# Performance work log

Hardware: AMD Instinct MI355X
Metric: run time of the kernel (lower is better)

The kernel has to match this reference:

```python
import jax, jax.numpy as jnp
import numpy as np
from jax import lax

N, C, H, W = 16, 512, 64, 64
INTER, HEADS, GROUPS, K = 512, 64, 8, 7
HEAD_DIM = INTER // HEADS


def setup_inputs() -> dict:
    key = jax.random.key(0)
    ks = jax.random.split(key, 12)
    s = 0.02
    return {
        "x": jax.random.normal(ks[0], (N, C, H, W), jnp.float32),
        "conv_w": jax.random.normal(ks[1], (INTER, C // GROUPS, K, K), jnp.float32) * s,
        "conv_b": jax.random.normal(ks[2], (INTER,), jnp.float32) * s,
        "ln_g": jnp.ones((INTER,), jnp.float32),
        "ln_b": jnp.zeros((INTER,), jnp.float32),
        "qw": jax.random.normal(ks[3], (INTER, INTER), jnp.float32) * s,
        "qb": jax.random.normal(ks[4], (INTER,), jnp.float32) * s,
        "kw": jax.random.normal(ks[5], (INTER, INTER), jnp.float32) * s,
        "kb": jax.random.normal(ks[6], (INTER,), jnp.float32) * s,
        "vw": jax.random.normal(ks[7], (INTER, INTER), jnp.float32) * s,
        "vb": jax.random.normal(ks[8], (INTER,), jnp.float32) * s,
        "pw": jax.random.normal(ks[9], (C, INTER), jnp.float32) * s,
        "pb": jax.random.normal(ks[10], (C,), jnp.float32) * s,
        "beta": jax.random.normal(ks[11], (1,), jnp.float32),
    }


def reference(x, conv_w, conv_b, ln_g, ln_b, qw, qb, kw, kb, vw, vb, pw, pb, beta):
    n, c, h, w = x.shape
    hw = h * w
    pad = (K - 1) // 2
    # grouped conv, NCHW
    xc = lax.conv_general_dilated(
        x, conv_w, window_strides=(1, 1), padding=[(pad, pad), (pad, pad)],
        dimension_numbers=("NCHW", "OIHW", "NCHW"), feature_group_count=GROUPS)
    xc = xc + conv_b[None, :, None, None]
    xc = xc.reshape(n, INTER, hw).transpose(0, 2, 1)  # [N, HW, INTER]
    # LayerNorm over channel dim
    mu = jnp.mean(xc, axis=-1, keepdims=True)
    var = jnp.mean(jnp.square(xc - mu), axis=-1, keepdims=True)
    xn = (xc - mu) * lax.rsqrt(var + 1e-5) * ln_g + ln_b
    # projections (torch Linear: y = x @ W.T + b)
    q = (xn @ qw.T + qb).reshape(n, hw, HEADS, HEAD_DIM).transpose(0, 2, 1, 3)  # [N,h,HW,d]
    k = (xn @ kw.T + kb).reshape(n, hw, HEADS, HEAD_DIM).transpose(0, 2, 3, 1)  # [N,h,d,HW]
    v = (xn @ vw.T + vb).reshape(n, hw, HEADS, HEAD_DIM).transpose(0, 2, 1, 3)  # [N,h,HW,d]
    k = jax.nn.softmax(k, axis=3)  # softmax over tokens
    corr = jnp.einsum("nhds,nhse->nhde", k, v)      # [N,h,d,d] compact context
    atten = jnp.einsum("nhsd,nhde->nhse", q, corr)  # [N,h,HW,d]
    atten = atten.transpose(0, 2, 1, 3).reshape(n, hw, INTER)
    xa = (atten @ pw.T + pb).transpose(0, 2, 1).reshape(n, c, h, w)
    return beta[0] * xa + x
```

## Files before the change

### kernel.cpp

```cpp
#include <hip/hip_runtime.h>
#include <hip/hip_bf16.h>

#define N_IMG 16
#define C_DIM 512
#define H_DIM 64
#define W_DIM 64
#define HW 4096
#define INTER 512
#define HEADS 64
#define GROUPS 8
#define KSZ 7
#define CPG 64
#define M_TOT (N_IMG * HW)

typedef short bf16x8 __attribute__((ext_vector_type(8)));
typedef short bf16x4 __attribute__((ext_vector_type(4)));
typedef float f32x4 __attribute__((ext_vector_type(4)));
typedef unsigned int u32;

__device__ __forceinline__ unsigned short f2bf(float f) {
    __hip_bfloat16 h = __float2bfloat16(f);
    return *reinterpret_cast<unsigned short*>(&h);
}
__device__ __forceinline__ float bf2f(unsigned short u) {
    u32 x = ((u32)u) << 16;
    union { u32 i; float f; } c; c.i = x; return c.f;
}
__device__ __forceinline__ void gload16(const void* g, void* l) {
    __builtin_amdgcn_global_load_lds(
        (const __attribute__((address_space(1))) u32*)g,
        (__attribute__((address_space(3))) u32*)l, 16, 0, 0);
}

__global__ __launch_bounds__(256) void zero_kernel(float* __restrict__ p)
{
    p[blockIdx.x * 256 + threadIdx.x] = 0.f;
}

__global__ __launch_bounds__(256) void wpack_kernel(
    const float* __restrict__ cw, unsigned short* __restrict__ pk)
{
    int p = blockIdx.x * 256 + threadIdx.x;
    int ci = p & 63;
    int co = (p >> 6) & 63;
    int r  = p >> 12;
    int dx = r % 7;
    int dyg = r / 7;
    int dy = dyg % 7;
    int g  = dyg / 7;
    float v = cw[(((size_t)(g * 64 + co)) * 64 + ci) * 49 + dy * 7 + dx];
    pk[(size_t)(g * 49 + dy * 7 + dx) * 4096 + co * 64 + (ci ^ ((co & 7) << 3))] = f2bf(v);
}

__global__ __launch_bounds__(256) void wpack_proj_kernel(
    const float* __restrict__ w, unsigned short* __restrict__ wp)
{
    int e = blockIdx.x * 256 + threadIdx.x;
    int j = e & 7;
    int chunk = (e >> 3) & 511;
    int kt = (e >> 12) & 15;
    int t = e >> 16;
    int col = chunk & 127, kq = chunk >> 7;
    wp[e] = f2bf(w[(size_t)(t * 128 + col) * 512 + kt * 32 + kq * 8 + j]);
}

__global__ __launch_bounds__(256) void pwcast_kernel(
    const float* __restrict__ w, unsigned short* __restrict__ wb)
{
    int i = blockIdx.x * 256 + threadIdx.x;
    wb[i] = f2bf(w[i]);
}

__global__ __launch_bounds__(256) void xprep_kernel(
    const float* __restrict__ x, unsigned short* __restrict__ xb)
{
    const int row = blockIdx.x;
    const int g   = blockIdx.y;
    const int n   = blockIdx.z;
    const int tid = threadIdx.x;
    unsigned short* dst = xb + ((size_t)(n * 8 + g) * 70 + row) * 4608;

    if (row < 3 || row > 66) {
        bf16x8 z = (bf16x8){0,0,0,0,0,0,0,0};
        *(bf16x8*)&dst[tid * 8] = z;
        *(bf16x8*)&dst[(256 + tid) * 8] = z;
        if (tid < 64) *(bf16x8*)&dst[(512 + tid) * 8] = z;
        return;
    }
    const int y = row - 3;
    const int xcol = tid & 63;
    const int oct = tid >> 6;
    const int col = xcol + 3;
    const int cswz = (col & 7) << 3;
    const float* src = x + (((size_t)(n * C_DIM + g * CPG)) * H_DIM + y) * W_DIM + xcol;
#pragma unroll
    for (int h = 0; h < 2; ++h) {
        const int ci0 = oct * 16 + h * 8;
        unsigned short tmp[8];
#pragma unroll
        for (int j = 0; j < 8; ++j)
            tmp[j] = f2bf(src[(size_t)(ci0 + j) * (H_DIM * W_DIM)]);
        *(bf16x8*)&dst[col * 64 + (ci0 ^ cswz)] = *(bf16x8*)tmp;
    }
    if (tid < 64) {
        const int hc[8] = {0, 1, 2, 67, 68, 69, 70, 71};
        int c = hc[tid >> 3], o8 = (tid & 7) * 8;
        *(bf16x8*)&dst[c * 64 + (o8 ^ ((c & 7) << 3))] = (bf16x8){0,0,0,0,0,0,0,0};
    }
}

__global__ __launch_bounds__(256) void conv_mfma2_kernel(
    const unsigned short* __restrict__ xb, const unsigned short* __restrict__ pk,
    const float* __restrict__ cb, unsigned short* __restrict__ xc)
{
    __shared__ __align__(16) unsigned short in_ring[4 * 72 * 64];
    __shared__ __align__(16) unsigned short w_lds[2 * 4096];

    const int bid  = blockIdx.x;
    const int wgid = (bid & 7) * 256 + (bid >> 3);
    const int g  = wgid >> 8;
    const int n  = (wgid >> 4) & 15;
    const int y0 = (wgid & 15) * 4;
    const int tid  = threadIdx.x;
    const int lane = tid & 63;
    const int wv   = tid >> 6;
    const int lx   = lane & 15;
    const int q4   = lane >> 4;
    const int koff = q4 * 8;

    const unsigned short* xbase = xb + ((size_t)(n * 8 + g) * 70) * 4608;
    const unsigned short* pkg   = pk + (size_t)g * 49 * 4096;

    f32x4 acc[4][4];
#pragma unroll
    for (int i = 0; i < 4; ++i)
#pragma unroll
        for (int j = 0; j < 4; ++j) acc[i][j] = (f32x4){0.f, 0.f, 0.f, 0.f};

#pragma unroll
    for (int r = 0; r < 4; ++r) {
        const unsigned short* src = xbase + (size_t)(y0 + r) * 4608;
        gload16(src + tid * 8,         &in_ring[r * 4608 + tid * 8]);
        gload16(src + (256 + tid) * 8, &in_ring[r * 4608 + (256 + tid) * 8]);
        if (tid < 64)
            gload16(src + (512 + tid) * 8, &in_ring[r * 4608 + (512 + tid) * 8]);
    }
    gload16(pkg + tid * 8,         &w_lds[tid * 8]);
    gload16(pkg + (256 + tid) * 8, &w_lds[(256 + tid) * 8]);
    __syncthreads();

    for (int dy = 0; dy < 7; ++dy) {
        if (dy > 0) {
            const int slot = (dy + 3) & 3;
            const unsigned short* src = xbase + (size_t)(y0 + dy + 3) * 4608;
            gload16(src + tid * 8,         &in_ring[slot * 4608 + tid * 8]);
            gload16(src + (256 + tid) * 8, &in_ring[slot * 4608 + (256 + tid) * 8]);
            if (tid < 64)
                gload16(src + (512 + tid) * 8, &in_ring[slot * 4608 + (512 + tid) * 8]);
            __syncthreads();
        }
#pragma unroll
        for (int dx = 0; dx < 7; ++dx) {
            const int t = dy * 7 + dx;
            if (t < 48) {
                const unsigned short* wsrc = pkg + (size_t)(t + 1) * 4096;
                unsigned short* wdst = &w_lds[((t + 1) & 1) * 4096];
                gload16(wsrc + tid * 8,         wdst + tid * 8);
                gload16(wsrc + (256 + tid) * 8, wdst + (256 + tid) * 8);
            }
            const unsigned short* wcur = &w_lds[(t & 1) * 4096];
            bf16x8 b[2][4];
#pragma unroll
            for (int kc = 0; kc < 2; ++kc)
#pragma unroll
                for (int ct = 0; ct < 4; ++ct) {
                    const int co = ct * 16 + lx;
                    b[kc][ct] = *(const bf16x8*)
                        &wcur[co * 64 + ((kc * 32 + koff) ^ ((co & 7) << 3))];
                }
            const int col  = wv * 16 + lx + dx;
            const int cswz = (col & 7) << 3;
#pragma unroll
            for (int ty = 0; ty < 4; ++ty) {
                const int slot = (dy + ty) & 3;
#pragma unroll
                for (int kc = 0; kc < 2; ++kc) {
                    bf16x8 a = *(const bf16x8*)
                        &in_ring[slot * 4608 + col * 64 + ((kc * 32 + koff) ^ cswz)];
#pragma unroll
                    for (int ct = 0; ct < 4; ++ct)
                        acc[ty][ct] = __builtin_amdgcn_mfma_f32_16x16x32_bf16(
                            a, b[kc][ct], acc[ty][ct], 0, 0, 0);
                }
            }
            __syncthreads();
        }
    }

#pragma unroll
    for (int ct = 0; ct < 4; ++ct) {
        const float bv = cb[g * 64 + ct * 16 + lx];
        const int cidx = g * 64 + ct * 16 + lx;
#pragma unroll
        for (int ty = 0; ty < 4; ++ty) {
            const int yy = y0 + ty;
#pragma unroll
            for (int r = 0; r < 4; ++r) {
                const int xx = wv * 16 + q4 * 4 + r;
                xc[((size_t)(n * HW + yy * W_DIM + xx)) * INTER + cidx]
                    = f2bf(acc[ty][ct][r] + bv);
            }
        }
    }
}

__global__ __launch_bounds__(256) void ln_kernel(
    unsigned short* __restrict__ xc, const float* __restrict__ g,
    const float* __restrict__ b)
{
    const int tid  = threadIdx.x;
    const int half = tid >> 7;
    const int l    = tid & 127;
    const size_t row = (size_t)blockIdx.x * 2 + half;

    bf16x4 u = *(const bf16x4*)(xc + row * INTER + l * 4);
    float v0 = bf2f((unsigned short)u[0]), v1 = bf2f((unsigned short)u[1]);
    float v2 = bf2f((unsigned short)u[2]), v3 = bf2f((unsigned short)u[3]);
    float s  = v0 + v1 + v2 + v3;
    float sq = v0 * v0 + v1 * v1 + v2 * v2 + v3 * v3;
#pragma unroll
    for (int off = 32; off; off >>= 1) {
        s  += __shfl_xor(s, off);
        sq += __shfl_xor(sq, off);
    }
    __shared__ float red[4][2];
    const int wid = tid >> 6;
    if ((tid & 63) == 0) { red[wid][0] = s; red[wid][1] = sq; }
    __syncthreads();
    const int w0 = half * 2;
    float S  = red[w0][0] + red[w0 + 1][0];
    float SQ = red[w0][1] + red[w0 + 1][1];
    float mu  = S * (1.f / INTER);
    float var = SQ * (1.f / INTER) - mu * mu;
    float rs  = rsqrtf(var + 1e-5f);
    float4 gg = ((const float4*)g)[l];
    float4 bb = ((const float4*)b)[l];
    bf16x4 o;
    o[0] = (short)f2bf((v0 - mu) * rs * gg.x + bb.x);
    o[1] = (short)f2bf((v1 - mu) * rs * gg.y + bb.y);
    o[2] = (short)f2bf((v2 - mu) * rs * gg.z + bb.z);
    o[3] = (short)f2bf((v3 - mu) * rs * gg.w + bb.w);
    *(bf16x4*)(xc + row * INTER + l * 4) = o;
}

__global__ __launch_bounds__(256, 2) void gemm_kv_corr_kernel(
    const unsigned short* __restrict__ A,
    const unsigned short* __restrict__ Wk, const unsigned short* __restrict__ Wv,
    const float* __restrict__ bk, const float* __restrict__ bv,
    float* __restrict__ crw, float* __restrict__ esw)
{
    __shared__ __align__(16) unsigned short pool[32768];
    unsigned short* ek_lds = pool;
    unsigned short* v_lds  = pool + 16384;

    const int tid  = threadIdx.x;
    const int lane = tid & 63;
    const int w    = tid >> 6;
    const int lx   = lane & 15;
    const int kq4  = lane >> 4;

    const int orig = blockIdx.x;
    const int wgid = (orig & 7) * 256 + (orig >> 3);
    const int m0   = (wgid >> 2) * 128;
    const int ct4  = wgid & 3;
    const int mbase = (w & 1) * 64;
    const int nbase = (w >> 1) * 64;
    const int n = m0 >> 12;

    const unsigned short* wkt = Wk + (size_t)ct4 * 65536;
    const unsigned short* wvt = Wv + (size_t)ct4 * 65536;

    f32x4 acck[4][4], accv[4][4];
#pragma unroll
    for (int i = 0; i < 4; ++i)
#pragma unroll
        for (int j = 0; j < 4; ++j) {
            acck[i][j] = (f32x4){0.f, 0.f, 0.f, 0.f};
            accv[i][j] = (f32x4){0.f, 0.f, 0.f, 0.f};
        }

#pragma unroll
    for (int it = 0; it < 2; ++it) {
        int c = it * 256 + tid;
        gload16(A + (size_t)(m0 + (c & 127)) * 512 + (c >> 7) * 8, &pool[c * 8]);
        gload16(wkt + c * 8, &pool[(1024 + c) * 8]);
        gload16(wvt + c * 8, &pool[(2048 + c) * 8]);
    }
    __syncthreads();

    for (int kt = 0; kt < 16; ++kt) {
        const int b = kt & 1;
        if (kt < 15) {
            const int nb = b ^ 1;
#pragma unroll
            for (int it = 0; it < 2; ++it) {
                int c = it * 256 + tid;
                gload16(A + (size_t)(m0 + (c & 127)) * 512 + (kt + 1) * 32 + (c >> 7) * 8,
                        &pool[(nb * 512 + c) * 8]);
                gload16(wkt + (size_t)(kt + 1) * 4096 + c * 8, &pool[(1024 + nb * 512 + c) * 8]);
                gload16(wvt + (size_t)(kt + 1) * 4096 + c * 8, &pool[(2048 + nb * 512 + c) * 8]);
            }
        }
        bf16x8 a[4], bkf[4], bvf[4];
#pragma unroll
        for (int i = 0; i < 4; ++i) {
            a[i]   = *(const bf16x8*)&pool[(b * 512 + kq4 * 128 + mbase + i * 16 + lx) * 8];
            bkf[i] = *(const bf16x8*)&pool[(1024 + b * 512 + kq4 * 128 + nbase + i * 16 + lx) * 8];
            bvf[i] = *(const bf16x8*)&pool[(2048 + b * 512 + kq4 * 128 + nbase + i * 16 + lx) * 8];
        }
#pragma unroll
        for (int i = 0; i < 4; ++i)
#pragma unroll
            for (int j = 0; j < 4; ++j) {
                acck[i][j] = __builtin_amdgcn_mfma_f32_16x16x32_bf16(a[i], bkf[j], acck[i][j], 0, 0, 0);
                accv[i][j] = __builtin_amdgcn_mfma_f32_16x16x32_bf16(a[i], bvf[j], accv[i][j], 0, 0, 0);
            }
        __syncthreads();
    }

#pragma unroll
    for (int j = 0; j < 4; ++j) {
        const int colk = nbase + j * 16 + lx;
        const float bkv = bk[ct4 * 128 + colk];
        const float bvv = bv[ct4 * 128 + colk];
        const int sw = (colk & 7) << 3;
#pragma unroll
        for (int i = 0; i < 4; ++i) {
            const int t0 = mbase + i * 16 + kq4 * 4;
            const int idx = colk * 128 + (t0 ^ sw);
            bf16x4 ew, vw;
#pragma unroll
            for (int r = 0; r < 4; ++r) {
                ew[r] = (short)f2bf(__expf(acck[i][j][r] + bkv));
                vw[r] = (short)f2bf(accv[i][j][r] + bvv);
            }
            *(bf16x4*)&ek_lds[idx] = ew;
            *(bf16x4*)&v_lds[idx]  = vw;
        }
    }
    const int d = lane >> 3, e = lane & 7;
    const int hbase = (w >> 1) * 8;
#pragma unroll
    for (int h = 0; h < 8; ++h) {
        const int hb = hbase + h;
        const int ck = hb * 8 + d;
        const int ce = hb * 8 + e;
        const int swk = d << 3, swe = e << 3;
        float crh = 0.f, esh = 0.f;
#pragma unroll
        for (int tb = 0; tb < 16; ++tb) {
            const int t0 = mbase + tb * 4;
            bf16x4 ekv = *(const bf16x4*)&ek_lds[ck * 128 + (t0 ^ swk)];
            bf16x4 vvv = *(const bf16x4*)&v_lds[ce * 128 + (t0 ^ swe)];
#pragma unroll
            for (int r = 0; r < 4; ++r) {
                float ekf = bf2f((unsigned short)ekv[r]);
                crh = fmaf(ekf, bf2f((unsigned short)vvv[r]), crh);
                esh += ekf;
            }
        }
        const int nh = n * 64 + ct4 * 16 + hb;
        atomicAdd(&crw[(size_t)nh * 64 + d * 8 + e], crh);
        if (e == 0) atomicAdd(&esw[nh * 8 + d], esh);
    }
}

__global__ __launch_bounds__(256) void norm_corr_kernel(
    const float* __restrict__ crw, const float* __restrict__ esw,
    float* __restrict__ corr)
{
    int idx = blockIdx.x * 256 + threadIdx.x;
    int nh = idx >> 6, d = (idx >> 3) & 7;
    corr[idx] = crw[idx] / esw[nh * 8 + d];
}

__global__ __launch_bounds__(256) void gcomp_kernel(
    const float* __restrict__ qw, const float* __restrict__ corr,
    unsigned short* __restrict__ G)
{
    const int h = blockIdx.x;
    const int n = blockIdx.y;
    const int tid = threadIdx.x;
    __shared__ float C[64];
    if (tid < 64) C[tid] = corr[((size_t)(n * 64 + h)) * 64 + tid];
    __syncthreads();
#pragma unroll
    for (int rep = 0; rep < 2; ++rep) {
        const int k = rep * 256 + tid;
        float o[8] = {};
#pragma unroll
        for (int d = 0; d < 8; ++d) {
            float qv = qw[(size_t)(h * 8 + d) * 512 + k];
#pragma unroll
            for (int e = 0; e < 8; ++e) o[e] = fmaf(qv, C[d * 8 + e], o[e]);
        }
        bf16x8 ov;
#pragma unroll
        for (int e = 0; e < 8; ++e) ov[e] = (short)f2bf(o[e]);
        *(bf16x8*)&G[((size_t)n * 512 + k) * 512 + h * 8] = ov;
    }
}

__global__ __launch_bounds__(256) void compose_kernel(
    const unsigned short* __restrict__ Pwb, const unsigned short* __restrict__ G,
    unsigned short* __restrict__ Wf)
{
    __shared__ __align__(16) unsigned short pool[16384];
    const int tid  = threadIdx.x;
    const int lane = tid & 63;
    const int w    = tid >> 6;
    const int lx   = lane & 15;
    const int kq4  = lane >> 4;

    const int tile = blockIdx.x;
    const int n    = blockIdx.y;
    const int m0 = (tile >> 2) * 128;
    const int n0 = (tile & 3) * 128;
    const int mbase = (w & 1) * 64;
    const int nbase = (w >> 1) * 64;
    const unsigned short* Gn = G + (size_t)n * 262144;

    f32x4 acc[4][4];
#pragma unroll
    for (int i = 0; i < 4; ++i)
#pragma unroll
        for (int j = 0; j < 4; ++j) acc[i][j] = (f32x4){0.f, 0.f, 0.f, 0.f};

#pragma unroll
    for (int it = 0; it < 2; ++it) {
        int c = it * 256 + tid;
        gload16(Pwb + (size_t)(m0 + (c & 127)) * 512 + (c >> 7) * 8, &pool[c * 8]);
        gload16(Gn + (size_t)(n0 + (c & 127)) * 512 + (c >> 7) * 8, &pool[(1024 + c) * 8]);
    }
    __syncthreads();

    for (int kt = 0; kt < 16; ++kt) {
        const int b = kt & 1;
        if (kt < 15) {
            const int nb = b ^ 1;
#pragma unroll
            for (int it = 0; it < 2; ++it) {
                int c = it * 256 + tid;
                gload16(Pwb + (size_t)(m0 + (c & 127)) * 512 + (kt + 1) * 32 + (c >> 7) * 8,
                        &pool[(nb * 512 + c) * 8]);
                gload16(Gn + (size_t)(n0 + (c & 127)) * 512 + (kt + 1) * 32 + (c >> 7) * 8,
                        &pool[(1024 + nb * 512 + c) * 8]);
            }
        }
        bf16x8 a[4], bf[4];
#pragma unroll
        for (int i = 0; i < 4; ++i) {
            a[i]  = *(const bf16x8*)&pool[(b * 512 + kq4 * 128 + mbase + i * 16 + lx) * 8];
            bf[i] = *(const bf16x8*)&pool[(1024 + b * 512 + kq4 * 128 + nbase + i * 16 + lx) * 8];
        }
#pragma unroll
        for (int i = 0; i < 4; ++i)
#pragma unroll
            for (int j = 0; j < 4; ++j)
                acc[i][j] = __builtin_amdgcn_mfma_f32_16x16x32_bf16(a[i], bf[j], acc[i][j], 0, 0, 0);
        __syncthreads();
    }

#pragma unroll
    for (int j = 0; j < 4; ++j) {
        const int col = n0 + nbase + j * 16 + lx;
#pragma unroll
        for (int i = 0; i < 4; ++i) {
            const int rowb = m0 + mbase + i * 16 + kq4 * 4;
#pragma unroll
            for (int r = 0; r < 4; ++r)
                Wf[(size_t)n * 262144 + (size_t)(rowb + r) * 512 + col] = f2bf(acc[i][j][r]);
        }
    }
}

__global__ __launch_bounds__(256) void wfpack_kernel(
    const unsigned short* __restrict__ Wf, unsigned short* __restrict__ wfp)
{
    const int n = blockIdx.y;
    int e = blockIdx.x * 256 + threadIdx.x;
    int j = e & 7;
    int chunk = (e >> 3) & 511;
    int kt = (e >> 12) & 15;
    int t = e >> 16;
    int col = chunk & 127, kq = chunk >> 7;
    wfp[(size_t)n * 262144 + e] =
        Wf[(size_t)n * 262144 + (size_t)(t * 128 + col) * 512 + kt * 32 + kq * 8 + j];
}

__global__ __launch_bounds__(256) void bias2_kernel(
    const float* __restrict__ qb, const float* __restrict__ corr,
    const float* __restrict__ pw, const float* __restrict__ pb,
    float* __restrict__ b2)
{
    const int n = blockIdx.x;
    const int tid = threadIdx.x;
    __shared__ float qbc[512];
#pragma unroll
    for (int rep = 0; rep < 2; ++rep) {
        int j = rep * 256 + tid;
        int h = j >> 3, e = j & 7;
        float s = 0.f;
#pragma unroll
        for (int d = 0; d < 8; ++d)
            s += qb[h * 8 + d] * corr[((size_t)(n * 64 + h)) * 64 + d * 8 + e];
        qbc[j] = s;
    }
    __syncthreads();
#pragma unroll
    for (int rep = 0; rep < 2; ++rep) {
        int c = rep * 256 + tid;
        const float4* pr = (const float4*)(pw + (size_t)c * 512);
        float s = pb[c];
        for (int q = 0; q < 128; ++q) {
            float4 pv = pr[q];
            s += qbc[q * 4 + 0] * pv.x + qbc[q * 4 + 1] * pv.y
               + qbc[q * 4 + 2] * pv.z + qbc[q * 4 + 3] * pv.w;
        }
        b2[n * 512 + c] = s;
    }
}

__global__ __launch_bounds__(256) void gemm_p_kernel(
    const unsigned short* __restrict__ A, const unsigned short* __restrict__ Wp,
    const float* __restrict__ bias, float* __restrict__ Y,
    const float* __restrict__ xres, const float* __restrict__ betap)
{
    __shared__ __align__(16) unsigned short pool[24576];
    const int tid  = threadIdx.x;
    const int lane = tid & 63;
    const int w    = tid >> 6;
    const int lx   = lane & 15;
    const int kq4  = lane >> 4;

    const int orig = blockIdx.x;
    const int wgid = (orig & 7) * 128 + (orig >> 3);
    const int m0 = (wgid >> 2) * 256;
    const int n0 = (wgid & 3) * 128;
    const int mbase = (w & 1) * 128;
    const int nbase = (w >> 1) * 64;
    const int nimg = m0 >> 12;

    f32x4 acc[8][4];
#pragma unroll
    for (int i = 0; i < 8; ++i)
#pragma unroll
        for (int j = 0; j < 4; ++j) acc[i][j] = (f32x4){0.f, 0.f, 0.f, 0.f};

    const unsigned short* wpt = Wp + (size_t)nimg * 262144 + (size_t)(wgid & 3) * 65536;

#pragma unroll
    for (int it = 0; it < 4; ++it) {
        int c = it * 256 + tid;
        gload16(A + (size_t)(m0 + (c & 255)) * 512 + (c >> 8) * 8, &pool[c * 8]);
    }
#pragma unroll
    for (int it = 0; it < 2; ++it) {
        int c = it * 256 + tid;
        gload16(wpt + c * 8, &pool[16384 + c * 8]);
    }
    __syncthreads();

    for (int kt = 0; kt < 16; ++kt) {
        const int b = kt & 1;
        if (kt < 15) {
            const int nb = b ^ 1;
#pragma unroll
            for (int it = 0; it < 4; ++it) {
                int c = it * 256 + tid;
                gload16(A + (size_t)(m0 + (c & 255)) * 512 + (kt + 1) * 32 + (c >> 8) * 8,
                        &pool[(nb * 1024 + c) * 8]);
            }
#pragma unroll
            for (int it = 0; it < 2; ++it) {
                int c = it * 256 + tid;
                gload16(wpt + (size_t)(kt + 1) * 4096 + c * 8,
                        &pool[16384 + (nb * 512 + c) * 8]);
            }
        }
        bf16x8 a[8], bf[4];
#pragma unroll
        for (int i = 0; i < 8; ++i)
            a[i] = *(const bf16x8*)&pool[(b * 1024 + kq4 * 256 + mbase + i * 16 + lx) * 8];
#pragma unroll
        for (int j = 0; j < 4; ++j)
            bf[j] = *(const bf16x8*)&pool[16384 + (b * 512 + kq4 * 128 + nbase + j * 16 + lx) * 8];
#pragma unroll
        for (int i = 0; i < 8; ++i)
#pragma unroll
            for (int j = 0; j < 4; ++j)
                acc[i][j] = __builtin_amdgcn_mfma_f32_16x16x32_bf16(a[i], bf[j], acc[i][j], 0, 0, 0);
        __syncthreads();
    }

    const float beta = betap[0];
#pragma unroll
    for (int j = 0; j < 4; ++j) {
        const int c = n0 + nbase + j * 16 + lx;
        const float pbv = bias[nimg * 512 + c];
        const size_t cbase = ((size_t)(nimg * 512 + c)) * 4096;
#pragma unroll
        for (int i = 0; i < 8; ++i) {
            const int s = (m0 & 4095) + mbase + i * 16 + kq4 * 4;
            float4 xr = *(const float4*)(xres + cbase + s);
            float4 o;
            o.x = beta * (acc[i][j][0] + pbv) + xr.x;
            o.y = beta * (acc[i][j][1] + pbv) + xr.y;
            o.z = beta * (acc[i][j][2] + pbv) + xr.z;
            o.w = beta * (acc[i][j][3] + pbv) + xr.w;
            *(float4*)(Y + cbase + s) = o;
        }
    }
}

extern "C" void kernel_launch(void* const* d_in, const int* in_sizes, int n_in,
                              void* d_out, int out_size, void* d_ws, size_t ws_size,
                              hipStream_t stream)
{
    (void)in_sizes; (void)n_in; (void)out_size; (void)ws_size;
    const float* x   = (const float*)d_in[0];
    const float* cw  = (const float*)d_in[1];
    const float* cb  = (const float*)d_in[2];
    const float* lng = (const float*)d_in[3];
    const float* lnb = (const float*)d_in[4];
    const float* qw  = (const float*)d_in[5];
    const float* qb  = (const float*)d_in[6];
    const float* kw  = (const float*)d_in[7];
    const float* kb  = (const float*)d_in[8];
    const float* vw  = (const float*)d_in[9];
    const float* vb  = (const float*)d_in[10];
    const float* pw  = (const float*)d_in[11];
    const float* pb  = (const float*)d_in[12];
    const float* beta = (const float*)d_in[13];
    float* out = (float*)d_out;

    char* ws = (char*)d_ws;
    const size_t SZ  = (size_t)M_TOT * INTER * sizeof(float);
    const size_t HSZ = (size_t)M_TOT * INTER * 2;
    unsigned short* xc   = (unsigned short*)ws;
    unsigned short* G    = (unsigned short*)(ws + HSZ);
    unsigned short* wfin = G + (size_t)16 * 262144;
    unsigned short* wfp  = wfin + (size_t)16 * 262144;
    unsigned short* pwb  = wfp + (size_t)16 * 262144;
    float* b2            = (float*)(pwb + 262144);
    float* crw  = (float*)(ws + SZ);
    float* esw  = crw + 65536;
    float* corr = (float*)(ws + SZ + (1 << 20));
    unsigned short* pk  = (unsigned short*)(ws + SZ + (2 << 20));
    unsigned short* kwb = (unsigned short*)(ws + SZ + (6 << 20));
    unsigned short* vwb = kwb + 262144;
    unsigned short* xb  = vwb + 262144;

    zero_kernel<<<dim3(288), 256, 0, stream>>>(crw);
    wpack_kernel<<<dim3(6272), 256, 0, stream>>>(cw, pk);
    wpack_proj_kernel<<<dim3(1024), 256, 0, stream>>>(kw, kwb);
    wpack_proj_kernel<<<dim3(1024), 256, 0, stream>>>(vw, vwb);
    pwcast_kernel<<<dim3(1024), 256, 0, stream>>>(pw, pwb);
    xprep_kernel<<<dim3(70, 8, 16), 256, 0, stream>>>(x, xb);

    conv_mfma2_kernel<<<dim3(2048), 256, 0, stream>>>(xb, pk, cb, xc);
    ln_kernel<<<dim3(M_TOT / 2), 256, 0, stream>>>(xc, lng, lnb);

    gemm_kv_corr_kernel<<<dim3(2048), 256, 0, stream>>>(xc, kwb, vwb, kb, vb, crw, esw);
    norm_corr_kernel<<<dim3(256), 256, 0, stream>>>(crw, esw, corr);

    gcomp_kernel<<<dim3(64, 16), 256, 0, stream>>>(qw, corr, G);
    compose_kernel<<<dim3(16, 16), 256, 0, stream>>>(pwb, G, wfin);
    wfpack_kernel<<<dim3(1024, 16), 256, 0, stream>>>(wfin, wfp);
    bias2_kernel<<<dim3(16), 256, 0, stream>>>(qb, corr, pw, pb, b2);

    gemm_p_kernel<<<dim3(1024), 256, 0, stream>>>(xc, wfp, b2, out, x, beta);
}
```

Measured before the change: 522.8 us.

## Merge prep kernels, fold corr normalization, and use explicit vmcnt barriers

Five weight-packing and zeroing kernels become one launch, and the separate corr normalization kernel is folded into its consumers (gcomp and bias2), which cuts launch count. In the conv and both GEMM loops, __syncthreads is replaced by raw s_barrier plus explicit s_waitcnt vmcnt counts. This lets the next tile's global-to-LDS loads stay in flight across the barrier instead of draining every iteration. The conv loop now issues its third row load unconditionally, writing into the 64-entry tail region of each ring slot. The hand-counted vmcnt values are fragile and could cause races if the instruction count changes.

```diff
diff --git a/kernel.cpp b/kernel.cpp
--- a/kernel.cpp
+++ b/kernel.cpp
@@ -31,44 +31,49 @@
         (const __attribute__((address_space(1))) u32*)g,
         (__attribute__((address_space(3))) u32*)l, 16, 0, 0);
 }
-
-__global__ __launch_bounds__(256) void zero_kernel(float* __restrict__ p)
-{
-    p[blockIdx.x * 256 + threadIdx.x] = 0.f;
-}
-
-__global__ __launch_bounds__(256) void wpack_kernel(
-    const float* __restrict__ cw, unsigned short* __restrict__ pk)
-{
-    int p = blockIdx.x * 256 + threadIdx.x;
-    int ci = p & 63;
-    int co = (p >> 6) & 63;
-    int r  = p >> 12;
-    int dx = r % 7;
-    int dyg = r / 7;
-    int dy = dyg % 7;
-    int g  = dyg / 7;
-    float v = cw[(((size_t)(g * 64 + co)) * 64 + ci) * 49 + dy * 7 + dx];
-    pk[(size_t)(g * 49 + dy * 7 + dx) * 4096 + co * 64 + (ci ^ ((co & 7) << 3))] = f2bf(v);
-}
-
-__global__ __launch_bounds__(256) void wpack_proj_kernel(
-    const float* __restrict__ w, unsigned short* __restrict__ wp)
-{
-    int e = blockIdx.x * 256 + threadIdx.x;
-    int j = e & 7;
-    int chunk = (e >> 3) & 511;
-    int kt = (e >> 12) & 15;
-    int t = e >> 16;
-    int col = chunk & 127, kq = chunk >> 7;
-    wp[e] = f2bf(w[(size_t)(t * 128 + col) * 512 + kt * 32 + kq * 8 + j]);
-}
-
-__global__ __launch_bounds__(256) void pwcast_kernel(
-    const float* __restrict__ w, unsigned short* __restrict__ wb)
-{
-    int i = blockIdx.x * 256 + threadIdx.x;
-    wb[i] = f2bf(w[i]);
+__device__ __forceinline__ void raw_barrier() {
+    asm volatile("" ::: "memory");
+    __builtin_amdgcn_s_barrier();
+    asm volatile("" ::: "memory");
+}
+#define WAIT_VM(N) asm volatile("s_waitcnt vmcnt(" #N ")" ::: "memory")
+
+__global__ __launch_bounds__(256) void prep_kernel(
+    const float* __restrict__ cw, const float* __restrict__ kw,
+    const float* __restrict__ vw, const float* __restrict__ pw,
+    unsigned short* __restrict__ pk, unsigned short* __restrict__ kwb,
+    unsigned short* __restrict__ vwb, unsigned short* __restrict__ pwb,
+    float* __restrict__ crw)
+{
+    const int b = blockIdx.x;
+    const int tid = threadIdx.x;
+    if (b < 6272) {
+        int p = b * 256 + tid;
+        int ci = p & 63;
+        int co = (p >> 6) & 63;
+        int r  = p >> 12;
+        int dx = r % 7;
+        int dyg = r / 7;
+        int dy = dyg % 7;
+        int g  = dyg / 7;
+        float v = cw[(((size_t)(g * 64 + co)) * 64 + ci) * 49 + dy * 7 + dx];
+        pk[(size_t)(g * 49 + dy * 7 + dx) * 4096 + co * 64 + (ci ^ ((co & 7) << 3))] = f2bf(v);
+    } else if (b < 8320) {
+        const float* w = (b < 7296) ? kw : vw;
+        unsigned short* wp = (b < 7296) ? kwb : vwb;
+        int e = ((b < 7296) ? (b - 6272) : (b - 7296)) * 256 + tid;
+        int j = e & 7;
+        int chunk = (e >> 3) & 511;
+        int kt = (e >> 12) & 15;
+        int t = e >> 16;
+        int col = chunk & 127, kq = chunk >> 7;
+        wp[e] = f2bf(w[(size_t)(t * 128 + col) * 512 + kt * 32 + kq * 8 + j]);
+    } else if (b < 9344) {
+        int i = (b - 8320) * 256 + tid;
+        pwb[i] = f2bf(pw[i]);
+    } else {
+        crw[(b - 9344) * 256 + tid] = 0.f;
+    }
 }
 
 __global__ __launch_bounds__(256) void xprep_kernel(
@@ -127,6 +132,7 @@
     const int lx   = lane & 15;
     const int q4   = lane >> 4;
     const int koff = q4 * 8;
+    const int c3   = 512 + (tid & 63);
 
     const unsigned short* xbase = xb + ((size_t)(n * 8 + g) * 70) * 4608;
     const unsigned short* pkg   = pk + (size_t)g * 49 * 4096;
@@ -142,32 +148,36 @@
         const unsigned short* src = xbase + (size_t)(y0 + r) * 4608;
         gload16(src + tid * 8,         &in_ring[r * 4608 + tid * 8]);
         gload16(src + (256 + tid) * 8, &in_ring[r * 4608 + (256 + tid) * 8]);
-        if (tid < 64)
-            gload16(src + (512 + tid) * 8, &in_ring[r * 4608 + (512 + tid) * 8]);
+        gload16(src + c3 * 8,          &in_ring[r * 4608 + c3 * 8]);
     }
     gload16(pkg + tid * 8,         &w_lds[tid * 8]);
     gload16(pkg + (256 + tid) * 8, &w_lds[(256 + tid) * 8]);
-    __syncthreads();
 
     for (int dy = 0; dy < 7; ++dy) {
-        if (dy > 0) {
-            const int slot = (dy + 3) & 3;
-            const unsigned short* src = xbase + (size_t)(y0 + dy + 3) * 4608;
-            gload16(src + tid * 8,         &in_ring[slot * 4608 + tid * 8]);
-            gload16(src + (256 + tid) * 8, &in_ring[slot * 4608 + (256 + tid) * 8]);
-            if (tid < 64)
-                gload16(src + (512 + tid) * 8, &in_ring[slot * 4608 + (512 + tid) * 8]);
-            __syncthreads();
-        }
 #pragma unroll
         for (int dx = 0; dx < 7; ++dx) {
             const int t = dy * 7 + dx;
+            raw_barrier();
+            if (dx == 0 && dy > 0) {
+                const int slot = (dy + 3) & 3;
+                const unsigned short* src = xbase + (size_t)(y0 + dy + 3) * 4608;
+                gload16(src + tid * 8,         &in_ring[slot * 4608 + tid * 8]);
+                gload16(src + (256 + tid) * 8, &in_ring[slot * 4608 + (256 + tid) * 8]);
+                gload16(src + c3 * 8,          &in_ring[slot * 4608 + c3 * 8]);
+            }
             if (t < 48) {
                 const unsigned short* wsrc = pkg + (size_t)(t + 1) * 4096;
                 unsigned short* wdst = &w_lds[((t + 1) & 1) * 4096];
                 gload16(wsrc + tid * 8,         wdst + tid * 8);
                 gload16(wsrc + (256 + tid) * 8, wdst + (256 + tid) * 8);
-            }
+                WAIT_VM(2);
+            } else {
+                WAIT_VM(0);
+            }
+            __builtin_amdgcn_sched_barrier(0);
+            raw_barrier();
+            __builtin_amdgcn_sched_barrier(0);
+
             const unsigned short* wcur = &w_lds[(t & 1) * 4096];
             bf16x8 b[2][4];
 #pragma unroll
@@ -193,7 +203,6 @@
                             a, b[kc][ct], acc[ty][ct], 0, 0, 0);
                 }
             }
-            __syncthreads();
         }
     }
 
@@ -296,7 +305,6 @@
         gload16(wkt + c * 8, &pool[(1024 + c) * 8]);
         gload16(wvt + c * 8, &pool[(2048 + c) * 8]);
     }
-    __syncthreads();
 
     for (int kt = 0; kt < 16; ++kt) {
         const int b = kt & 1;
@@ -310,7 +318,14 @@
                 gload16(wkt + (size_t)(kt + 1) * 4096 + c * 8, &pool[(1024 + nb * 512 + c) * 8]);
                 gload16(wvt + (size_t)(kt + 1) * 4096 + c * 8, &pool[(2048 + nb * 512 + c) * 8]);
             }
-        }
+            WAIT_VM(6);
+        } else {
+            WAIT_VM(0);
+        }
+        __builtin_amdgcn_sched_barrier(0);
+        raw_barrier();
+        __builtin_amdgcn_sched_barrier(0);
+
         bf16x8 a[4], bkf[4], bvf[4];
 #pragma unroll
         for (int i = 0; i < 4; ++i) {
@@ -325,7 +340,7 @@
                 acck[i][j] = __builtin_amdgcn_mfma_f32_16x16x32_bf16(a[i], bkf[j], acck[i][j], 0, 0, 0);
                 accv[i][j] = __builtin_amdgcn_mfma_f32_16x16x32_bf16(a[i], bvf[j], accv[i][j], 0, 0, 0);
             }
-        __syncthreads();
+        raw_barrier();
     }
 
 #pragma unroll
@@ -375,24 +390,16 @@
     }
 }
 
-__global__ __launch_bounds__(256) void norm_corr_kernel(
-    const float* __restrict__ crw, const float* __restrict__ esw,
-    float* __restrict__ corr)
-{
-    int idx = blockIdx.x * 256 + threadIdx.x;
-    int nh = idx >> 6, d = (idx >> 3) & 7;
-    corr[idx] = crw[idx] / esw[nh * 8 + d];
-}
-
 __global__ __launch_bounds__(256) void gcomp_kernel(
-    const float* __restrict__ qw, const float* __restrict__ corr,
-    unsigned short* __restrict__ G)
+    const float* __restrict__ qw, const float* __restrict__ crw,
+    const float* __restrict__ esw, unsigned short* __restrict__ G)
 {
     const int h = blockIdx.x;
     const int n = blockIdx.y;
     const int tid = threadIdx.x;
+    const int nh = n * 64 + h;
     __shared__ float C[64];
-    if (tid < 64) C[tid] = corr[((size_t)(n * 64 + h)) * 64 + tid];
+    if (tid < 64) C[tid] = crw[(size_t)nh * 64 + tid] / esw[nh * 8 + (tid >> 3)];
     __syncthreads();
 #pragma unroll
     for (int rep = 0; rep < 2; ++rep) {
@@ -499,9 +506,9 @@
 }
 
 __global__ __launch_bounds__(256) void bias2_kernel(
-    const float* __restrict__ qb, const float* __restrict__ corr,
-    const float* __restrict__ pw, const float* __restrict__ pb,
-    float* __restrict__ b2)
+    const float* __restrict__ qb, const float* __restrict__ crw,
+    const float* __restrict__ esw, const float* __restrict__ pw,
+    const float* __restrict__ pb, float* __restrict__ b2)
 {
     const int n = blockIdx.x;
     const int tid = threadIdx.x;
@@ -510,10 +517,11 @@
     for (int rep = 0; rep < 2; ++rep) {
         int j = rep * 256 + tid;
         int h = j >> 3, e = j & 7;
+        const int nh = n * 64 + h;
         float s = 0.f;
 #pragma unroll
         for (int d = 0; d < 8; ++d)
-            s += qb[h * 8 + d] * corr[((size_t)(n * 64 + h)) * 64 + d * 8 + e];
+            s += qb[h * 8 + d] * crw[(size_t)nh * 64 + d * 8 + e] / esw[nh * 8 + d];
         qbc[j] = s;
     }
     __syncthreads();
@@ -569,7 +577,6 @@
         int c = it * 256 + tid;
         gload16(wpt + c * 8, &pool[16384 + c * 8]);
     }
-    __syncthreads();
 
     for (int kt = 0; kt < 16; ++kt) {
         const int b = kt & 1;
@@ -587,7 +594,14 @@
                 gload16(wpt + (size_t)(kt + 1) * 4096 + c * 8,
                         &pool[16384 + (nb * 512 + c) * 8]);
             }
-        }
+            WAIT_VM(6);
+        } else {
+            WAIT_VM(0);
+        }
+        __builtin_amdgcn_sched_barrier(0);
+        raw_barrier();
+        __builtin_amdgcn_sched_barrier(0);
+
         bf16x8 a[8], bf[4];
 #pragma unroll
         for (int i = 0; i < 8; ++i)
@@ -600,7 +614,7 @@
 #pragma unroll
             for (int j = 0; j < 4; ++j)
                 acc[i][j] = __builtin_amdgcn_mfma_f32_16x16x32_bf16(a[i], bf[j], acc[i][j], 0, 0, 0);
-        __syncthreads();
+        raw_barrier();
     }
 
     const float beta = betap[0];
@@ -655,29 +669,23 @@
     float* b2            = (float*)(pwb + 262144);
     float* crw  = (float*)(ws + SZ);
     float* esw  = crw + 65536;
-    float* corr = (float*)(ws + SZ + (1 << 20));
     unsigned short* pk  = (unsigned short*)(ws + SZ + (2 << 20));
     unsigned short* kwb = (unsigned short*)(ws + SZ + (6 << 20));
     unsigned short* vwb = kwb + 262144;
     unsigned short* xb  = vwb + 262144;
 
-    zero_kernel<<<dim3(288), 256, 0, stream>>>(crw);
-    wpack_kernel<<<dim3(6272), 256, 0, stream>>>(cw, pk);
-    wpack_proj_kernel<<<dim3(1024), 256, 0, stream>>>(kw, kwb);
-    wpack_proj_kernel<<<dim3(1024), 256, 0, stream>>>(vw, vwb);
-    pwcast_kernel<<<dim3(1024), 256, 0, stream>>>(pw, pwb);
+    prep_kernel<<<dim3(9632), 256, 0, stream>>>(cw, kw, vw, pw, pk, kwb, vwb, pwb, crw);
     xprep_kernel<<<dim3(70, 8, 16), 256, 0, stream>>>(x, xb);
 
     conv_mfma2_kernel<<<dim3(2048), 256, 0, stream>>>(xb, pk, cb, xc);
     ln_kernel<<<dim3(M_TOT / 2), 256, 0, stream>>>(xc, lng, lnb);
 
     gemm_kv_corr_kernel<<<dim3(2048), 256, 0, stream>>>(xc, kwb, vwb, kb, vb, crw, esw);
-    norm_corr_kernel<<<dim3(256), 256, 0, stream>>>(crw, esw, corr);
-
-    gcomp_kernel<<<dim3(64, 16), 256, 0, stream>>>(qw, corr, G);
+
+    gcomp_kernel<<<dim3(64, 16), 256, 0, stream>>>(qw, crw, esw, G);
     compose_kernel<<<dim3(16, 16), 256, 0, stream>>>(pwb, G, wfin);
     wfpack_kernel<<<dim3(1024, 16), 256, 0, stream>>>(wfin, wfp);
-    bias2_kernel<<<dim3(16), 256, 0, stream>>>(qb, corr, pw, pb, b2);
+    bias2_kernel<<<dim3(16), 256, 0, stream>>>(qb, crw, esw, pw, pb, b2);
 
     gemm_p_kernel<<<dim3(1024), 256, 0, stream>>>(xc, wfp, b2, out, x, beta);
 }
```

Measured after the change: 507.5 us. 2.9% less time.
